# Performance work log

Measured on AMD Instinct MI355X. Metric: run time of the kernel, lower is better.

The kernel has to match this reference:

```python
import jax, jax.numpy as jnp
import numpy as np

B, S, H, NH, DH, FF, R, NE, EI, NT = 8, 1024, 768, 12, 64, 3072, 64, 512, 4096, 8
EPS = 1e-5


def layer_norm(x, g, b):
    m = jnp.mean(x, axis=-1, keepdims=True)
    v = jnp.var(x, axis=-1, keepdims=True)
    return (x - m) * jax.lax.rsqrt(v + EPS) * g + b


def adapter_apply(h, node_idx, edge_idx, types, dw, db, uw, ub, temb):
    """Hypergraph adapter: bottleneck down-proj, node->hyperedge mean gather,
    edge-type embedding, hyperedge->node mean scatter, up-proj. vmapped over batch."""
    def one(hb, nb, eb, tb):
        d = jax.nn.gelu(hb @ dw + db)                                  # [S, R]
        m = d[nb]                                                      # [EI, R] gather node feats per incidence
        ones = jnp.ones((EI,), d.dtype)
        esum = jax.ops.segment_sum(m, eb, num_segments=NE)             # [NE, R]
        ecnt = jax.ops.segment_sum(ones, eb, num_segments=NE)
        e = esum / jnp.maximum(ecnt, 1.0)[:, None] + temb[tb]          # hyperedge feats + type emb
        nsum = jax.ops.segment_sum(e[eb], nb, num_segments=S)          # scatter back to nodes
        ncnt = jax.ops.segment_sum(ones, nb, num_segments=S)
        u = nsum / jnp.maximum(ncnt, 1.0)[:, None]                     # [S, R]
        return u @ uw + ub                                             # [S, H]
    return jax.vmap(one)(h, node_idx, edge_idx, types)


def setup_inputs() -> dict:
    key = jax.random.key(0)
    ks = jax.random.split(key, 24)
    std = 0.02
    p = lambda k, shp: jax.random.normal(k, shp, jnp.float32) * std
    inp = {
        'hidden_states': jax.random.normal(ks[0], (B, S, H), jnp.float32),
        'node_idx': jax.random.randint(ks[1], (B, EI), 0, S, jnp.int32),
        'edge_idx': jax.random.randint(ks[2], (B, EI), 0, NE, jnp.int32),
        'edge_types': jax.random.randint(ks[3], (B, NE), 0, NT, jnp.int32),
        'Wq': p(ks[4], (H, H)), 'bq': jnp.zeros((H,), jnp.float32),
        'Wk': p(ks[5], (H, H)), 'bk': jnp.zeros((H,), jnp.float32),
        'Wv': p(ks[6], (H, H)), 'bv': jnp.zeros((H,), jnp.float32),
        'Wo': p(ks[7], (H, H)), 'bo': jnp.zeros((H,), jnp.float32),
        'ln1_g': jnp.ones((H,), jnp.float32), 'ln1_b': jnp.zeros((H,), jnp.float32),
        'a1_dw': p(ks[8], (H, R)), 'a1_db': jnp.zeros((R,), jnp.float32),
        'a1_uw': p(ks[9], (R, H)), 'a1_ub': jnp.zeros((H,), jnp.float32),
        'a1_temb': p(ks[10], (NT, R)),
        'Wi': p(ks[11], (H, FF)), 'bi': jnp.zeros((FF,), jnp.float32),
        'Wd2': p(ks[12], (FF, H)), 'bd2': jnp.zeros((H,), jnp.float32),
        'ln2_g': jnp.ones((H,), jnp.float32), 'ln2_b': jnp.zeros((H,), jnp.float32),
        'a2_dw': p(ks[13], (H, R)), 'a2_db': jnp.zeros((R,), jnp.float32),
        'a2_uw': p(ks[14], (R, H)), 'a2_ub': jnp.zeros((H,), jnp.float32),
        'a2_temb': p(ks[15], (NT, R)),
    }
    return inp


def reference(hidden_states, node_idx, edge_idx, edge_types,
              Wq, bq, Wk, bk, Wv, bv, Wo, bo, ln1_g, ln1_b,
              a1_dw, a1_db, a1_uw, a1_ub, a1_temb,
              Wi, bi, Wd2, bd2, ln2_g, ln2_b,
              a2_dw, a2_db, a2_uw, a2_ub, a2_temb):
    x = hidden_states
    # --- self attention ---
    q = (x @ Wq + bq).reshape(B, S, NH, DH)
    k = (x @ Wk + bk).reshape(B, S, NH, DH)
    v = (x @ Wv + bv).reshape(B, S, NH, DH)
    scores = jnp.einsum('bqhd,bkhd->bhqk', q, k) / jnp.sqrt(jnp.float32(DH))
    probs = jax.nn.softmax(scores, axis=-1)
    ctx = jnp.einsum('bhqk,bkhd->bqhd', probs, v).reshape(B, S, H)
    attn_dense = ctx @ Wo + bo                                         # dropout = identity (eval)
    # --- hypergraph adapter 1 + residual LN ---
    ad1 = adapter_apply(attn_dense, node_idx, edge_idx, edge_types, a1_dw, a1_db, a1_uw, a1_ub, a1_temb)
    attn_out = layer_norm(attn_dense + ad1 + x, ln1_g, ln1_b)
    # --- FFN ---
    inter = jax.nn.gelu(attn_out @ Wi + bi)
    ff = inter @ Wd2 + bd2
    # --- hypergraph adapter 2 + residual LN ---
    ad2 = adapter_apply(ff, node_idx, edge_idx, edge_types, a2_dw, a2_db, a2_uw, a2_ub, a2_temb)
    layer_output = layer_norm(ff + ad2 + attn_out, ln2_g, ln2_b)
    return layer_output
```

## Files before the change

kernel.cpp:

```cpp
#include <hip/hip_runtime.h>

typedef unsigned short u16;
typedef __attribute__((ext_vector_type(8))) short s16x8;
typedef __attribute__((ext_vector_type(4))) float f32x4;
typedef __attribute__((ext_vector_type(4))) unsigned short u16x4;

#define NB 8
#define SS 1024
#define HH 768
#define NHD 12
#define DHD 64
#define FFD 3072
#define RR 64
#define NEC 512
#define EIC 4096

__device__ __forceinline__ float b2f(u16 u){ return __uint_as_float(((unsigned)u)<<16); }
__device__ __forceinline__ u16 f2b(float f){
  unsigned x = __float_as_uint(f);
  return (u16)((x + 0x7fffu + ((x>>16)&1u)) >> 16);
}
__device__ __forceinline__ float gelu_f(float x){
  return 0.5f*x*(1.0f + tanhf(0.79788456080286535588f*(x + 0.044715f*x*x*x)));
}
__device__ __forceinline__ void xcd_swz(int gx, int gy, int& bx, int& by){
  const int nwg = gx*gy;
  const int flat = by*gx + bx;
  const int qch = nwg >> 3, rch = nwg & 7;
  const int xcd = flat & 7, idx = flat >> 3;
  const int swz = (xcd < rch ? xcd*(qch+1) : rch*(qch+1) + (xcd-rch)*qch) + idx;
  bx = swz % gx; by = swz / gx;
}

__global__ __launch_bounds__(256)
void cvt16(const float* __restrict__ src, u16* __restrict__ dst)
{
  const size_t i = ((size_t)blockIdx.x*256 + threadIdx.x)*8;
  float4 a = *(const float4*)&src[i];
  float4 b = *(const float4*)&src[i+4];
  u16x4 h1; h1.x=f2b(a.x); h1.y=f2b(a.y); h1.z=f2b(a.z); h1.w=f2b(a.w);
  u16x4 h2; h2.x=f2b(b.x); h2.y=f2b(b.y); h2.z=f2b(b.z); h2.w=f2b(b.w);
  *(u16x4*)&dst[i] = h1; *(u16x4*)&dst[i+4] = h2;
}

__global__ __launch_bounds__(256)
void wtrans(const float* __restrict__ src, u16* __restrict__ dst, int R, int C)
{
  __shared__ u16 tile[64][68];
  const int r0 = blockIdx.x*64, c0 = blockIdx.y*64;
  const int t = threadIdx.x;
  const int tr = t >> 4, tc = (t & 15) * 4;
  for (int i = 0; i < 4; i++) {
    int r = tr + i*16;
    float4 v4 = *(const float4*)&src[(size_t)(r0+r)*C + c0 + tc];
    u16x4 h; h.x = f2b(v4.x); h.y = f2b(v4.y); h.z = f2b(v4.z); h.w = f2b(v4.w);
    *(u16x4*)&tile[r][tc] = h;
  }
  __syncthreads();
  for (int i = 0; i < 4; i++) {
    int rr = tr + i*16;
    u16x4 v;
    v.x = tile[tc+0][rr]; v.y = tile[tc+1][rr];
    v.z = tile[tc+2][rr]; v.w = tile[tc+3][rr];
    *(u16x4*)&dst[(size_t)(c0+rr)*R + r0 + tc] = v;
  }
}

__global__ __launch_bounds__(256)
void vtrans(const u16* __restrict__ v, u16* __restrict__ vt, int vs)
{
  __shared__ u16 tile[64][68];
  const int st = blockIdx.x, bh = blockIdx.y;
  const int b = bh / NHD, h = bh - b*NHD;
  const u16* src = v + (size_t)(b*SS + st*64)*vs + h*DHD;
  u16* dst = vt + (size_t)bh*DHD*SS + st*64;
  const int t = threadIdx.x;
  const int tr = t >> 4, tc = (t & 15) * 4;
  for (int i = 0; i < 4; i++) {
    int r = tr + i*16;
    *(u16x4*)&tile[r][tc] = *(const u16x4*)&src[(size_t)r*vs + tc];
  }
  __syncthreads();
  for (int i = 0; i < 4; i++) {
    int rr = tr + i*16;
    u16x4 vv;
    vv.x = tile[tc+0][rr]; vv.y = tile[tc+1][rr];
    vv.z = tile[tc+2][rr]; vv.w = tile[tc+3][rr];
    *(u16x4*)&dst[(size_t)rr*SS + tc] = vv;
  }
}

template<int BM, int BN, int ACT, int OUT>
__global__ __launch_bounds__(256)
void gemm_bt(const u16* __restrict__ A, const u16* __restrict__ Bt,
             const float* __restrict__ bias, float* __restrict__ C32,
             u16* __restrict__ C16, int M, int N, int K)
{
  constexpr int MF = BM/32;
  constexpr int NF = BN/32;
  __shared__ __align__(16) u16 lsA[BM*64];
  __shared__ __align__(16) u16 lsB[BN*64];
  int bx = blockIdx.x, by = blockIdx.y;
  xcd_swz(gridDim.x, gridDim.y, bx, by);
  const int m0 = by*BM, n0 = bx*BN;
  const int t = threadIdx.x, lane = t & 63, w = t >> 6;
  const int wm = w >> 1, wn = w & 1;
  const int l15 = lane & 15, lg = lane >> 4;

  f32x4 acc[MF][NF];
  #pragma unroll
  for (int i = 0; i < MF; i++)
    #pragma unroll
    for (int j = 0; j < NF; j++) acc[i][j] = (f32x4){0.f,0.f,0.f,0.f};

  for (int k0 = 0; k0 < K; k0 += 64) {
    __syncthreads();
    #pragma unroll
    for (int i = 0; i < BM/32; i++) {
      const int p = (w*(BM/32) + i)*64 + lane;
      const int r = p >> 3;
      const int ch = (p & 7) ^ (r & 7);
      __builtin_amdgcn_global_load_lds(
        (const __attribute__((address_space(1))) unsigned*)(A + (size_t)(m0+r)*K + k0 + ch*8),
        (__attribute__((address_space(3))) unsigned*)(lsA + (w*(BM/32)+i)*512),
        16, 0, 0);
    }
    #pragma unroll
    for (int i = 0; i < BN/32; i++) {
      const int p = (w*(BN/32) + i)*64 + lane;
      const int r = p >> 3;
      const int ch = (p & 7) ^ (r & 7);
      __builtin_amdgcn_global_load_lds(
        (const __attribute__((address_space(1))) unsigned*)(Bt + (size_t)(n0+r)*K + k0 + ch*8),
        (__attribute__((address_space(3))) unsigned*)(lsB + (w*(BN/32)+i)*512),
        16, 0, 0);
    }
    __syncthreads();
    #pragma unroll
    for (int kk = 0; kk < 64; kk += 32) {
      const int cb = (kk >> 3) + lg;
      s16x8 af[MF], bfr[NF];
      #pragma unroll
      for (int i = 0; i < MF; i++) {
        const int row = wm*(BM/2) + i*16 + l15;
        af[i] = *(const s16x8*)&lsA[row*64 + ((cb ^ (row & 7)) << 3)];
      }
      #pragma unroll
      for (int j = 0; j < NF; j++) {
        const int row = wn*(BN/2) + j*16 + l15;
        bfr[j] = *(const s16x8*)&lsB[row*64 + ((cb ^ (row & 7)) << 3)];
      }
      #pragma unroll
      for (int i = 0; i < MF; i++)
        #pragma unroll
        for (int j = 0; j < NF; j++)
          acc[i][j] = __builtin_amdgcn_mfma_f32_16x16x32_bf16(af[i], bfr[j], acc[i][j], 0, 0, 0);
    }
  }
  #pragma unroll
  for (int j = 0; j < NF; j++) {
    const int col = n0 + wn*(BN/2) + j*16 + l15;
    const float bv = bias[col];
    #pragma unroll
    for (int i = 0; i < MF; i++) {
      #pragma unroll
      for (int r = 0; r < 4; r++) {
        const int row = m0 + wm*(BM/2) + i*16 + (lg << 2) + r;
        float v = acc[i][j][r] + bv;
        if (ACT == 1) v = gelu_f(v);
        if constexpr (OUT == 0 || OUT == 2) C32[(size_t)row*N + col] = v;
        if constexpr (OUT == 1 || OUT == 2) C16[(size_t)row*N + col] = f2b(v);
      }
    }
  }
}

__global__ __launch_bounds__(256)
void attn_fwd(const u16* __restrict__ q, const u16* __restrict__ k,
              const u16* __restrict__ vt, u16* __restrict__ ctx, int qs)
{
  int bx = blockIdx.x, by = blockIdx.y;
  xcd_swz(gridDim.x, gridDim.y, bx, by);
  const int qt = bx, bh = by;
  const int b = bh / NHD, h = bh - b*NHD;
  __shared__ __align__(16) u16 lsK[64][72];
  __shared__ __align__(16) u16 lsV[64][72];
  __shared__ __align__(16) u16 lsP[4][16][72];
  const int t = threadIdx.x, lane = t & 63, w = t >> 6;
  const int l15 = lane & 15, lg = lane >> 4;

  const int qrow = qt*64 + w*16 + l15;
  const size_t qoff = (size_t)(b*SS + qrow)*qs + h*DHD;
  const s16x8 qf0 = *(const s16x8*)&q[qoff + (lg << 3)];
  const s16x8 qf1 = *(const s16x8*)&q[qoff + 32 + (lg << 3)];

  float m_run = -1e30f, l_run = 0.f;
  f32x4 oacc[4];
  #pragma unroll
  for (int j = 0; j < 4; j++) oacc[j] = (f32x4){0.f,0.f,0.f,0.f};

  const u16* kbase = k + (size_t)(b*SS)*qs + h*DHD;
  const u16* vbase = vt + (size_t)bh*DHD*SS;

  for (int kt = 0; kt < SS/64; kt++) {
    __syncthreads();
    for (int c = t; c < 512; c += 256) {
      int r = c >> 3, cc = (c & 7) << 3;
      *(s16x8*)&lsK[r][cc] = *(const s16x8*)&kbase[(size_t)(kt*64 + r)*qs + cc];
    }
    for (int c = t; c < 512; c += 256) {
      int r = c >> 3, cc = (c & 7) << 3;
      *(s16x8*)&lsV[r][cc] = *(const s16x8*)&vbase[(size_t)r*SS + kt*64 + cc];
    }
    __syncthreads();

    f32x4 sc[4];
    #pragma unroll
    for (int mf = 0; mf < 4; mf++) sc[mf] = (f32x4){0.f,0.f,0.f,0.f};
    #pragma unroll
    for (int kk = 0; kk < 2; kk++) {
      const int ko = kk*32 + (lg << 3);
      const s16x8 qv = kk ? qf1 : qf0;
      #pragma unroll
      for (int mf = 0; mf < 4; mf++) {
        s16x8 kf = *(const s16x8*)&lsK[mf*16 + l15][ko];
        sc[mf] = __builtin_amdgcn_mfma_f32_16x16x32_bf16(kf, qv, sc[mf], 0, 0, 0);
      }
    }
    float pmax = sc[0][0];
    #pragma unroll
    for (int mf = 0; mf < 4; mf++)
      #pragma unroll
      for (int r = 0; r < 4; r++) pmax = fmaxf(pmax, sc[mf][r]);
    pmax *= 0.125f;
    pmax = fmaxf(pmax, __shfl_xor(pmax, 16, 64));
    pmax = fmaxf(pmax, __shfl_xor(pmax, 32, 64));
    const bool need = !__all(pmax - m_run <= 8.0f);
    const float nm = need ? fmaxf(m_run, pmax) : m_run;
    float sum = 0.f;
    #pragma unroll
    for (int mf = 0; mf < 4; mf++) {
      u16x4 ph;
      #pragma unroll
      for (int r = 0; r < 4; r++) {
        const float p = __expf(sc[mf][r]*0.125f - nm);
        sum += p;
        ph[r] = f2b(p);
      }
      *(u16x4*)&lsP[w][l15][mf*16 + (lg << 2)] = ph;
    }
    sum += __shfl_xor(sum, 16, 64);
    sum += __shfl_xor(sum, 32, 64);
    if (need) {
      const float alpha = __expf(m_run - nm);
      l_run = l_run*alpha + sum;
      m_run = nm;
      #pragma unroll
      for (int r = 0; r < 4; r++) {
        const float ar = __shfl(alpha, (lg << 2) + r, 64);
        #pragma unroll
        for (int j = 0; j < 4; j++) oacc[j][r] *= ar;
      }
    } else {
      l_run += sum;
    }
    #pragma unroll
    for (int ks = 0; ks < 2; ks++) {
      const int ko = ks*32 + (lg << 3);
      const s16x8 pf = *(const s16x8*)&lsP[w][l15][ko];
      #pragma unroll
      for (int j = 0; j < 4; j++) {
        s16x8 vf = *(const s16x8*)&lsV[j*16 + l15][ko];
        oacc[j] = __builtin_amdgcn_mfma_f32_16x16x32_bf16(pf, vf, oacc[j], 0, 0, 0);
      }
    }
  }
  const float linv = 1.f / l_run;
  #pragma unroll
  for (int r = 0; r < 4; r++) {
    const float lr = __shfl(linv, (lg << 2) + r, 64);
    #pragma unroll
    for (int j = 0; j < 4; j++) {
      const int row = qt*64 + w*16 + (lg << 2) + r;
      ctx[((size_t)(b*SS + row))*HH + h*DHD + j*16 + l15] = f2b(oacc[j][r] * lr);
    }
  }
}

__global__ __launch_bounds__(256)
void adp_gather(const float* __restrict__ d, const int* __restrict__ nidx,
                const int* __restrict__ eidx, float* __restrict__ esum,
                float* __restrict__ ecnt)
{
  const int gi = blockIdx.x*4 + (threadIdx.x >> 6);
  const int lane = threadIdx.x & 63;
  const int b = gi >> 12, i = gi & (EIC - 1);
  const int n = nidx[(size_t)b*EIC + i];
  const int e = eidx[(size_t)b*EIC + i];
  const float val = d[((size_t)b*SS + n)*RR + lane];
  atomicAdd(&esum[((size_t)b*NEC + e)*RR + lane], val);
  if (lane == 0) atomicAdd(&ecnt[(size_t)b*NEC + e], 1.0f);
}

__global__ __launch_bounds__(256)
void adp_edge(const float* __restrict__ esum, const float* __restrict__ ecnt,
              const int* __restrict__ types, const float* __restrict__ temb,
              float* __restrict__ e_out)
{
  const int ge = blockIdx.x*4 + (threadIdx.x >> 6);
  const int lane = threadIdx.x & 63;
  const int b = ge >> 9, e = ge & (NEC - 1);
  const float cnt = fmaxf(ecnt[(size_t)b*NEC + e], 1.0f);
  const int ty = types[(size_t)b*NEC + e];
  e_out[((size_t)b*NEC + e)*RR + lane] =
      esum[((size_t)b*NEC + e)*RR + lane]/cnt + temb[(size_t)ty*RR + lane];
}

__global__ __launch_bounds__(256)
void adp_scatter(const float* __restrict__ e_out, const int* __restrict__ nidx,
                 const int* __restrict__ eidx, float* __restrict__ nsum,
                 float* __restrict__ ncnt)
{
  const int gi = blockIdx.x*4 + (threadIdx.x >> 6);
  const int lane = threadIdx.x & 63;
  const int b = gi >> 12, i = gi & (EIC - 1);
  const int n = nidx[(size_t)b*EIC + i];
  const int e = eidx[(size_t)b*EIC + i];
  atomicAdd(&nsum[((size_t)b*SS + n)*RR + lane], e_out[((size_t)b*NEC + e)*RR + lane]);
  if (lane == 0) atomicAdd(&ncnt[(size_t)b*SS + n], 1.0f);
}

__global__ __launch_bounds__(256)
void adp_node(const float* __restrict__ nsum, const float* __restrict__ ncnt,
              u16* __restrict__ u)
{
  const int gn = blockIdx.x*4 + (threadIdx.x >> 6);
  const int lane = threadIdx.x & 63;
  const float cnt = fmaxf(ncnt[gn], 1.0f);
  u[(size_t)gn*RR + lane] = f2b(nsum[(size_t)gn*RR + lane]/cnt);
}

__global__ __launch_bounds__(256)
void ln3(const float* __restrict__ a, const float* __restrict__ bb,
         const float* __restrict__ c, const float* __restrict__ g,
         const float* __restrict__ be, float* __restrict__ out,
         u16* __restrict__ outb)
{
  const int row = blockIdx.x, t = threadIdx.x;
  const size_t base = (size_t)row*HH;
  float v[3]; float s = 0.f, s2 = 0.f;
  #pragma unroll
  for (int i = 0; i < 3; i++) {
    int col = t + i*256;
    float x = a[base+col] + bb[base+col] + c[base+col];
    v[i] = x; s += x; s2 += x*x;
  }
  #pragma unroll
  for (int o = 1; o < 64; o <<= 1) { s += __shfl_xor(s, o, 64); s2 += __shfl_xor(s2, o, 64); }
  __shared__ float red[2][4];
  if ((t & 63) == 0) { red[0][t>>6] = s; red[1][t>>6] = s2; }
  __syncthreads();
  const float S  = red[0][0]+red[0][1]+red[0][2]+red[0][3];
  const float S2 = red[1][0]+red[1][1]+red[1][2]+red[1][3];
  const float mean = S*(1.0f/HH);
  const float var  = S2*(1.0f/HH) - mean*mean;
  const float inv  = rsqrtf(var + 1e-5f);
  #pragma unroll
  for (int i = 0; i < 3; i++) {
    int col = t + i*256;
    const float res = (v[i]-mean)*inv*g[col] + be[col];
    out[base+col] = res;
    if (outb) outb[base+col] = f2b(res);
  }
}

extern "C" void kernel_launch(void* const* d_in, const int* in_sizes, int n_in,
                              void* d_out, int out_size, void* d_ws, size_t ws_size,
                              hipStream_t stream)
{
  (void)in_sizes; (void)n_in; (void)out_size; (void)ws_size;
  const float* x        = (const float*)d_in[0];
  const int* node_idx   = (const int*)d_in[1];
  const int* edge_idx   = (const int*)d_in[2];
  const int* edge_types = (const int*)d_in[3];
  const float* Wq = (const float*)d_in[4];  const float* bq = (const float*)d_in[5];
  const float* Wk = (const float*)d_in[6];  const float* bk = (const float*)d_in[7];
  const float* Wv = (const float*)d_in[8];  const float* bv = (const float*)d_in[9];
  const float* Wo = (const float*)d_in[10]; const float* bo = (const float*)d_in[11];
  const float* ln1_g = (const float*)d_in[12]; const float* ln1_b = (const float*)d_in[13];
  const float* a1_dw = (const float*)d_in[14]; const float* a1_db = (const float*)d_in[15];
  const float* a1_uw = (const float*)d_in[16]; const float* a1_ub = (const float*)d_in[17];
  const float* a1_temb = (const float*)d_in[18];
  const float* Wi  = (const float*)d_in[19]; const float* bi  = (const float*)d_in[20];
  const float* Wd2 = (const float*)d_in[21]; const float* bd2 = (const float*)d_in[22];
  const float* ln2_g = (const float*)d_in[23]; const float* ln2_b = (const float*)d_in[24];
  const float* a2_dw = (const float*)d_in[25]; const float* a2_db = (const float*)d_in[26];
  const float* a2_uw = (const float*)d_in[27]; const float* a2_ub = (const float*)d_in[28];
  const float* a2_temb = (const float*)d_in[29];

  char* ws = (char*)d_ws;
  size_t off = 0;
  auto take = [&](size_t bytes) -> size_t {
    size_t o = off; off += (bytes + 255) & ~(size_t)255; return o;
  };
  const size_t actB2 = (size_t)8192*768*2;
  const size_t actB4 = (size_t)8192*768*4;
  const size_t oWqkvT = take(2304ull*768*2);
  const size_t oWoT   = take(768ull*768*2);
  const size_t oWiT   = take(768ull*3072*2);
  const size_t oWd2T  = take(768ull*3072*2);
  const size_t oA1dwT = take(768ull*64*2);
  const size_t oA1uwT = take(768ull*64*2);
  const size_t oA2dwT = take(768ull*64*2);
  const size_t oA2uwT = take(768ull*64*2);
  const size_t oBqkv  = take(2304ull*4);
  const size_t oXbf  = take(actB2);
  const size_t oQkv  = take((size_t)8192*2304*2);
  const size_t oVt   = take(actB2);
  const size_t oCtx  = take(actB2);
  const size_t oAD   = take(actB4);
  const size_t oAdp  = take(actB4);
  const size_t oAO   = take(actB4);
  const size_t oAOb  = take(actB2);
  const size_t oDb   = take((size_t)8192*64*4);
  const size_t oUb   = take((size_t)8192*64*2);
  const size_t oEsum = take((size_t)8*512*64*4);
  const size_t oEcnt = take((size_t)8*512*4);
  const size_t oNsum = take((size_t)8*1024*64*4);
  const size_t oNcnt = take((size_t)8*1024*4);
  const size_t oEbuf = take((size_t)8*512*64*4);
  const size_t oInter = oQkv;
  const size_t oFF    = oAD;
  const size_t oFFb   = oCtx;
  const size_t oADb   = oXbf;
  const size_t zeroBytes = oEbuf - oEsum;

  u16* WqkvT = (u16*)(ws+oWqkvT); u16* WoT = (u16*)(ws+oWoT);
  u16* WiT = (u16*)(ws+oWiT);     u16* Wd2T = (u16*)(ws+oWd2T);
  u16* A1dwT = (u16*)(ws+oA1dwT); u16* A1uwT = (u16*)(ws+oA1uwT);
  u16* A2dwT = (u16*)(ws+oA2dwT); u16* A2uwT = (u16*)(ws+oA2uwT);
  float* bias_qkv = (float*)(ws+oBqkv);
  u16* xbf = (u16*)(ws+oXbf);
  u16* qkv = (u16*)(ws+oQkv);
  u16* vtb = (u16*)(ws+oVt);  u16* ctx = (u16*)(ws+oCtx);
  float* attn_dense = (float*)(ws+oAD); u16* attn_dense_bf = (u16*)(ws+oADb);
  float* adb = (float*)(ws+oAdp);
  float* attn_out = (float*)(ws+oAO);   u16* attn_out_bf = (u16*)(ws+oAOb);
  float* dbuf = (float*)(ws+oDb);       u16* ubuf = (u16*)(ws+oUb);
  float* esum = (float*)(ws+oEsum); float* ecnt = (float*)(ws+oEcnt);
  float* nsum = (float*)(ws+oNsum); float* ncnt = (float*)(ws+oNcnt);
  float* ebuf = (float*)(ws+oEbuf);
  u16* inter = (u16*)(ws+oInter);
  float* ffb = (float*)(ws+oFF);  u16* ffb_bf = (u16*)(ws+oFFb);

  const dim3 blk(256);
  wtrans<<<dim3(12,12), blk, 0, stream>>>(Wq,  WqkvT,            768, 768);
  wtrans<<<dim3(12,12), blk, 0, stream>>>(Wk,  WqkvT + 768*768,  768, 768);
  wtrans<<<dim3(12,12), blk, 0, stream>>>(Wv,  WqkvT + 2*768*768,768, 768);
  wtrans<<<dim3(12,12), blk, 0, stream>>>(Wo,  WoT,  768, 768);
  wtrans<<<dim3(12,48), blk, 0, stream>>>(Wi,  WiT,  768, 3072);
  wtrans<<<dim3(48,12), blk, 0, stream>>>(Wd2, Wd2T, 3072, 768);
  wtrans<<<dim3(12,1),  blk, 0, stream>>>(a1_dw, A1dwT, 768, 64);
  wtrans<<<dim3(1,12),  blk, 0, stream>>>(a1_uw, A1uwT, 64, 768);
  wtrans<<<dim3(12,1),  blk, 0, stream>>>(a2_dw, A2dwT, 768, 64);
  wtrans<<<dim3(1,12),  blk, 0, stream>>>(a2_uw, A2uwT, 64, 768);
  hipMemcpyAsync(bias_qkv,        bq, 768*4, hipMemcpyDeviceToDevice, stream);
  hipMemcpyAsync(bias_qkv + 768,  bk, 768*4, hipMemcpyDeviceToDevice, stream);
  hipMemcpyAsync(bias_qkv + 1536, bv, 768*4, hipMemcpyDeviceToDevice, stream);
  cvt16<<<3072, blk, 0, stream>>>(x, xbf);
  gemm_bt<64,128,0,1><<<dim3(18,128), blk, 0, stream>>>(xbf, WqkvT, bias_qkv, nullptr, qkv, 8192, 2304, 768);
  vtrans<<<dim3(16,96), blk, 0, stream>>>(qkv + 1536, vtb, 2304);
  attn_fwd<<<dim3(16,96), blk, 0, stream>>>(qkv, qkv + 768, vtb, ctx, 2304);
  gemm_bt<64,128,0,2><<<dim3(6,128), blk, 0, stream>>>(ctx, WoT, bo, attn_dense, attn_dense_bf, 8192, 768, 768);
  gemm_bt<64,64,1,0><<<dim3(1,128), blk, 0, stream>>>(attn_dense_bf, A1dwT, a1_db, dbuf, nullptr, 8192, 64, 768);
  hipMemsetAsync(ws + oEsum, 0, zeroBytes, stream);
  adp_gather<<<8192, blk, 0, stream>>>(dbuf, node_idx, edge_idx, esum, ecnt);
  adp_edge<<<1024, blk, 0, stream>>>(esum, ecnt, edge_types, a1_temb, ebuf);
  adp_scatter<<<8192, blk, 0, stream>>>(ebuf, node_idx, edge_idx, nsum, ncnt);
  adp_node<<<2048, blk, 0, stream>>>(nsum, ncnt, ubuf);
  gemm_bt<64,128,0,0><<<dim3(6,128), blk, 0, stream>>>(ubuf, A1uwT, a1_ub, adb, nullptr, 8192, 768, 64);
  ln3<<<8192, blk, 0, stream>>>(attn_dense, adb, x, ln1_g, ln1_b, attn_out, attn_out_bf);
  gemm_bt<64,128,1,1><<<dim3(24,128), blk, 0, stream>>>(attn_out_bf, WiT, bi, nullptr, inter, 8192, 3072, 768);
  gemm_bt<64,128,0,2><<<dim3(6,128), blk, 0, stream>>>(inter, Wd2T, bd2, ffb, ffb_bf, 8192, 768, 3072);
  gemm_bt<64,64,1,0><<<dim3(1,128), blk, 0, stream>>>(ffb_bf, A2dwT, a2_db, dbuf, nullptr, 8192, 64, 768);
  hipMemsetAsync(ws + oEsum, 0, zeroBytes, stream);
  adp_gather<<<8192, blk, 0, stream>>>(dbuf, node_idx, edge_idx, esum, ecnt);
  adp_edge<<<1024, blk, 0, stream>>>(esum, ecnt, edge_types, a2_temb, ebuf);
  adp_scatter<<<8192, blk, 0, stream>>>(ebuf, node_idx, edge_idx, nsum, ncnt);
  adp_node<<<2048, blk, 0, stream>>>(nsum, ncnt, ubuf);
  gemm_bt<64,128,0,0><<<dim3(6,128), blk, 0, stream>>>(ubuf, A2uwT, a2_ub, adb, nullptr, 8192, 768, 64);
  ln3<<<8192, blk, 0, stream>>>(ffb, adb, attn_out, ln2_g, ln2_b, (float*)d_out, nullptr);
}
```

Measured before the change: 584.0 us.

## Load attention K/V tiles via direct global-to-LDS with XOR swizzle, exp2 softmax

The attention kernel now stages K and V tiles with global_load_lds (16-byte direct-to-LDS loads) instead of round-tripping through registers. The padded LDS arrays become unpadded 64x64 arrays with an XOR chunk swizzle, which is meant to avoid bank conflicts on MFMA fragment reads. The softmax exponent is rewritten as exp2 with a folded scale, and bf16 packing uses the hardware v_cvt_pk_bf16_f32 instruction. The changes rely on the swizzled load mapping matching the read indexing, and the packed convert rounds differently from the previous software rounding.

```diff
diff --git a/kernel.cpp b/kernel.cpp
--- a/kernel.cpp
+++ b/kernel.cpp
@@ -183,8 +183,8 @@
   xcd_swz(gridDim.x, gridDim.y, bx, by);
   const int qt = bx, bh = by;
   const int b = bh / NHD, h = bh - b*NHD;
-  __shared__ __align__(16) u16 lsK[64][72];
-  __shared__ __align__(16) u16 lsV[64][72];
+  __shared__ __align__(16) u16 lsK[64*64];
+  __shared__ __align__(16) u16 lsV[64*64];
   __shared__ __align__(16) u16 lsP[4][16][72];
   const int t = threadIdx.x, lane = t & 63, w = t >> 6;
   const int l15 = lane & 15, lg = lane >> 4;
@@ -204,13 +204,17 @@
 
   for (int kt = 0; kt < SS/64; kt++) {
     __syncthreads();
-    for (int c = t; c < 512; c += 256) {
-      int r = c >> 3, cc = (c & 7) << 3;
-      *(s16x8*)&lsK[r][cc] = *(const s16x8*)&kbase[(size_t)(kt*64 + r)*qs + cc];
-    }
-    for (int c = t; c < 512; c += 256) {
-      int r = c >> 3, cc = (c & 7) << 3;
-      *(s16x8*)&lsV[r][cc] = *(const s16x8*)&vbase[(size_t)r*SS + kt*64 + cc];
+    #pragma unroll
+    for (int i = 0; i < 2; i++) {
+      const int p = (w*2 + i)*64 + lane;
+      const int r = p >> 3;
+      const int ch = (p & 7) ^ (r & 7);
+      __builtin_amdgcn_global_load_lds(
+        (const __attribute__((address_space(1))) unsigned*)(kbase + (size_t)(kt*64 + r)*qs + ch*8),
+        (__attribute__((address_space(3))) unsigned*)(lsK + (w*2+i)*512), 16, 0, 0);
+      __builtin_amdgcn_global_load_lds(
+        (const __attribute__((address_space(1))) unsigned*)(vbase + (size_t)r*SS + kt*64 + ch*8),
+        (__attribute__((address_space(3))) unsigned*)(lsV + (w*2+i)*512), 16, 0, 0);
     }
     __syncthreads();
 
@@ -219,11 +223,12 @@
     for (int mf = 0; mf < 4; mf++) sc[mf] = (f32x4){0.f,0.f,0.f,0.f};
     #pragma unroll
     for (int kk = 0; kk < 2; kk++) {
-      const int ko = kk*32 + (lg << 3);
+      const int cb = kk*4 + lg;
       const s16x8 qv = kk ? qf1 : qf0;
       #pragma unroll
       for (int mf = 0; mf < 4; mf++) {
-        s16x8 kf = *(const s16x8*)&lsK[mf*16 + l15][ko];
+        const int row = mf*16 + l15;
+        s16x8 kf = *(const s16x8*)&lsK[row*64 + ((cb ^ (row & 7)) << 3)];
         sc[mf] = __builtin_amdgcn_mfma_f32_16x16x32_bf16(kf, qv, sc[mf], 0, 0, 0);
       }
     }
@@ -237,17 +242,21 @@
     pmax = fmaxf(pmax, __shfl_xor(pmax, 32, 64));
     const bool need = !__all(pmax - m_run <= 8.0f);
     const float nm = need ? fmaxf(m_run, pmax) : m_run;
+    const float c1 = 0.125f * 1.44269504088896f;
+    const float c2 = -nm * 1.44269504088896f;
     float sum = 0.f;
     #pragma unroll
     for (int mf = 0; mf < 4; mf++) {
-      u16x4 ph;
-      #pragma unroll
-      for (int r = 0; r < 4; r++) {
-        const float p = __expf(sc[mf][r]*0.125f - nm);
-        sum += p;
-        ph[r] = f2b(p);
-      }
-      *(u16x4*)&lsP[w][l15][mf*16 + (lg << 2)] = ph;
+      float p0 = exp2f(fmaf(sc[mf][0], c1, c2));
+      float p1 = exp2f(fmaf(sc[mf][1], c1, c2));
+      float p2 = exp2f(fmaf(sc[mf][2], c1, c2));
+      float p3 = exp2f(fmaf(sc[mf][3], c1, c2));
+      sum += (p0 + p1) + (p2 + p3);
+      unsigned r01, r23;
+      asm("v_cvt_pk_bf16_f32 %0, %1, %2" : "=v"(r01) : "v"(p0), "v"(p1));
+      asm("v_cvt_pk_bf16_f32 %0, %1, %2" : "=v"(r23) : "v"(p2), "v"(p3));
+      uint2 pk; pk.x = r01; pk.y = r23;
+      *(uint2*)&lsP[w][l15][mf*16 + (lg << 2)] = pk;
     }
     sum += __shfl_xor(sum, 16, 64);
     sum += __shfl_xor(sum, 32, 64);
@@ -266,11 +275,12 @@
     }
     #pragma unroll
     for (int ks = 0; ks < 2; ks++) {
-      const int ko = ks*32 + (lg << 3);
-      const s16x8 pf = *(const s16x8*)&lsP[w][l15][ko];
+      const int cb = ks*4 + lg;
+      const s16x8 pf = *(const s16x8*)&lsP[w][l15][ks*32 + (lg << 3)];
       #pragma unroll
       for (int j = 0; j < 4; j++) {
-        s16x8 vf = *(const s16x8*)&lsV[j*16 + l15][ko];
+        const int row = j*16 + l15;
+        s16x8 vf = *(const s16x8*)&lsV[row*64 + ((cb ^ (row & 7)) << 3)];
         oacc[j] = __builtin_amdgcn_mfma_f32_16x16x32_bf16(pf, vf, oacc[j], 0, 0, 0);
       }
     }
```

After: 569.0 us. -2.6%, faster.
